# Kernel tuning notes

Measured on AMD Instinct MI355X. Metric: run time of the kernel, lower is better.

## Reference

```python
import jax, jax.numpy as jnp
import numpy as np

DIM = 4096; H = 32; D = 128; EPS = 1e-5
BLOCK = 16
BD = 8; MAXB = 64                    # decode seqs, blocks per decode seq
PB = 2; PSEQ = 1024; TP = PB * PSEQ  # prefill: 2 seqs x 1024 tokens
TOK = TP + BD
NBLOCKS = BD * MAXB + TP // BLOCK    # 640
NEG = -1e30


def setup_inputs() -> dict:
    key = jax.random.key(0)
    ks = jax.random.split(key, 10)
    std = 0.02
    x = jax.random.normal(ks[0], (TOK, DIM), jnp.float32)
    key_heap = jax.random.normal(ks[1], (NBLOCKS, BLOCK, H, D), jnp.float32)
    val_heap = jax.random.normal(ks[2], (NBLOCKS, BLOCK, H, D), jnp.float32)
    # decode seq i owns blocks [i*MAXB, (i+1)*MAXB); context_len includes the new token
    ctx = jax.random.randint(ks[3], (BD,), 256, MAXB * BLOCK + 1).astype(jnp.int32)
    block_table = (jnp.arange(BD)[:, None] * MAXB + jnp.arange(MAXB)[None, :]).astype(jnp.int32)
    prefill_slots = BD * MAXB * BLOCK + jnp.arange(TP)      # prefill fills blocks after decode region
    decode_slots = jnp.arange(BD) * MAXB * BLOCK + (ctx - 1)  # newest-token slot per decode seq
    slot_mapping = jnp.concatenate([prefill_slots, decode_slots]).astype(jnp.int32)
    cu = (jnp.arange(PB + 1) * PSEQ).astype(jnp.int32)
    return dict(
        x=x, key_heap=key_heap, val_heap=val_heap,
        slot_mapping=slot_mapping, decode_block_table=block_table,
        decode_context_lens=ctx, prefill_cu_seqlens=cu,
        num_prefill_tokens=TP, prefill_max_seqlen=PSEQ, decode_max_seq_len=MAXB * BLOCK,
        norm1_w=1.0 + std * jax.random.normal(ks[4], (DIM,), jnp.float32),
        norm2_w=1.0 + std * jax.random.normal(ks[5], (DIM,), jnp.float32),
        w_qkv_w=std * jax.random.normal(ks[6], (3 * H * D, DIM), jnp.float32),
        wo_w=std * jax.random.normal(ks[7], (DIM, H * D), jnp.float32),
        w_gate_up_w=std * jax.random.normal(ks[8], (8 * DIM, DIM), jnp.float32),
        w2_w=std * jax.random.normal(ks[9], (DIM, 4 * DIM), jnp.float32),
    )


def _rmsnorm(x, w):
    return x * jax.lax.rsqrt(jnp.mean(x * x, -1, keepdims=True) + EPS) * w


def _forward(x, key_heap, val_heap, norm1_w, norm2_w, w_qkv_w, wo_w, w_gate_up_w, w2_w,
             slot_mapping, decode_block_table, decode_context_lens, prefill_cu_seqlens,
             num_prefill_tokens):
    T = x.shape[0]
    scale = 1.0 / np.sqrt(D)
    residual = x
    # fused norm1 -> QKV projection
    qkv = (_rmsnorm(x, norm1_w) @ w_qkv_w.T).reshape(T, 3, H, D)
    q, k, v = qkv[:, 0], qkv[:, 1], qkv[:, 2]
    # paged cache write (ops.reshape_and_cache)
    nb, bs = key_heap.shape[0], key_heap.shape[1]
    key_flat = key_heap.reshape(nb * bs, H, D).at[slot_mapping].set(k)
    val_flat = val_heap.reshape(nb * bs, H, D).at[slot_mapping].set(v)
    # prefill: varlen causal self-attention (flash_attn_varlen_func)
    Tp = num_prefill_tokens
    pos = jnp.arange(Tp)
    seg = jnp.searchsorted(prefill_cu_seqlens, pos, side='right') - 1
    mask = (seg[:, None] == seg[None, :]) & (pos[:, None] >= pos[None, :])  # [Tp,Tp]
    s = jnp.einsum('ihd,jhd->hij', q[:Tp], k[:Tp]) * scale
    attn_p = jnp.einsum('hij,jhd->ihd',
                        jax.nn.softmax(jnp.where(mask[None], s, NEG), -1), v[:Tp])
    # decode: paged attention over cached KV (ops.paged_attention_v2)
    kd = key_flat.reshape(nb, bs, H, D)[decode_block_table].reshape(BD, -1, H, D)
    vd = val_flat.reshape(nb, bs, H, D)[decode_block_table].reshape(BD, -1, H, D)
    L = kd.shape[1]
    sd = jnp.einsum('bhd,blhd->bhl', q[Tp:], kd) * scale
    dmask = jnp.arange(L)[None, :] < decode_context_lens[:, None]
    attn_d = jnp.einsum('bhl,blhd->bhd',
                        jax.nn.softmax(jnp.where(dmask[:, None, :], sd, NEG), -1), vd)
    attn = jnp.concatenate([attn_p.reshape(Tp, H * D), attn_d.reshape(BD, H * D)], 0)
    # MLP: wo + residual, norm2, SwiGLU, down-proj, residual
    h = attn @ wo_w.T + residual
    residual = h
    gu = _rmsnorm(h, norm2_w) @ w_gate_up_w.T
    g, u = jnp.split(gu, 2, -1)
    return (jax.nn.silu(g) * u) @ w2_w.T + residual


def reference(x, key_heap, val_heap, slot_mapping, decode_block_table, decode_context_lens,
              prefill_cu_seqlens, num_prefill_tokens, prefill_max_seqlen, decode_max_seq_len,
              norm1_w, norm2_w, w_qkv_w, wo_w, w_gate_up_w, w2_w):
    del prefill_max_seqlen, decode_max_seq_len  # kernel scheduling hints only
    return _forward(x, key_heap, val_heap, norm1_w, norm2_w, w_qkv_w, wo_w, w_gate_up_w, w2_w,
                    slot_mapping, decode_block_table, decode_context_lens, prefill_cu_seqlens,
                    num_prefill_tokens)
```

## Files before the change

kernel.cpp:

```cpp
#include <hip/hip_runtime.h>
#include <hip/hip_bf16.h>
#include <stdint.h>

#define DIMC   4096
#define HC     32
#define DC     128
#define TPC    2048
#define TOKC   2056
#define BDC    8
#define MAXBC  64
#define PSEQC  1024
#define QKVN   12288
#define FFNC   16384
#define PSCALE 0.08838834764831843f

typedef __attribute__((ext_vector_type(8))) short short8;
typedef __attribute__((ext_vector_type(4))) float f32x4;
typedef __attribute__((ext_vector_type(4))) unsigned short u16x4;
typedef __attribute__((ext_vector_type(8))) unsigned short u16x8;

__device__ inline unsigned short f2bf(float f) {
  union { float f; unsigned u; } v; v.f = f;
  unsigned r = v.u + 0x7FFFu + ((v.u >> 16) & 1u);
  return (unsigned short)(r >> 16);
}
__device__ inline float bf2f(unsigned short u) {
  union { unsigned u; float f; } v; v.u = ((unsigned)u) << 16;
  return v.f;
}
__device__ inline f32x4 mfma16(short8 a, short8 b, f32x4 c) {
  return __builtin_amdgcn_mfma_f32_16x16x32_bf16(a, b, c, 0, 0, 0);
}
__device__ inline void gload16(const void* g, void* l) {
  __builtin_amdgcn_global_load_lds(
      (const __attribute__((address_space(1))) void*)g,
      (__attribute__((address_space(3))) void*)l, 16, 0, 0);
}

__global__ __launch_bounds__(256) void cvt_w(
    const float* __restrict__ in, unsigned short* __restrict__ out, long n8)
{
  long i = (long)blockIdx.x * 256 + threadIdx.x;
  const long stride = (long)gridDim.x * 256;
  for (; i < n8; i += stride) {
    f32x4 a = ((const f32x4*)in)[2 * i];
    f32x4 b = ((const f32x4*)in)[2 * i + 1];
    u16x8 o;
#pragma unroll
    for (int j = 0; j < 4; ++j) { o[j] = f2bf(a[j]); o[j + 4] = f2bf(b[j]); }
    ((u16x8*)out)[i] = o;
  }
}

__global__ __launch_bounds__(256) void rmsnorm_k(
    const float* __restrict__ x, const float* __restrict__ w,
    unsigned short* __restrict__ out)
{
  const int row = blockIdx.x;
  const int tid = threadIdx.x;
  const f32x4* xr = (const f32x4*)(x + (size_t)row * DIMC);
  f32x4 v[4];
  float ss = 0.f;
#pragma unroll
  for (int i = 0; i < 4; ++i) {
    v[i] = xr[i * 256 + tid];
    ss += v[i][0]*v[i][0] + v[i][1]*v[i][1] + v[i][2]*v[i][2] + v[i][3]*v[i][3];
  }
  for (int off = 32; off; off >>= 1) ss += __shfl_xor(ss, off);
  __shared__ float sred[4];
  if ((tid & 63) == 0) sred[tid >> 6] = ss;
  __syncthreads();
  const float rms = rsqrtf((sred[0]+sred[1]+sred[2]+sred[3]) * (1.f/DIMC) + 1e-5f);
  const f32x4* wr = (const f32x4*)w;
#pragma unroll
  for (int i = 0; i < 4; ++i) {
    f32x4 wv = wr[i * 256 + tid];
    u16x4 o;
#pragma unroll
    for (int j = 0; j < 4; ++j) o[j] = f2bf(v[i][j] * rms * wv[j]);
    *(u16x4*)(out + (size_t)row * DIMC + (size_t)(i * 256 + tid) * 4) = o;
  }
}

template<int MODE, int SK>
__global__ __launch_bounds__(512, 2) void gemm8p(
    const unsigned short* __restrict__ A, const unsigned short* __restrict__ Bh,
    float* __restrict__ Cf, unsigned short* __restrict__ Cb,
    const float* __restrict__ Res, int M, int N, int K)
{
  __shared__ char ldsc[131072];
  const int tid = threadIdx.x;
  const int lane = tid & 63, wid = tid >> 6;
  const int wr = wid >> 2, wc = wid & 3;
  const int lhi = lane >> 4, llo = lane & 15;

  const int nM = (M + 255) >> 8;
  const int nN = N >> 8;
  const int nwg = gridDim.x, orig = blockIdx.x;
  const int qq = nwg >> 3, rr = nwg & 7;
  const int xcd = orig & 7, lid = orig >> 3;
  const int wgid = (xcd < rr ? xcd*(qq+1) : rr*(qq+1) + (xcd-rr)*qq) + lid;
  const int tiles = nM * nN;
  const int ks = wgid / tiles;
  const int tile = wgid % tiles;
  const int bm = (tile % nM) << 8;
  const int bn = (tile / nM) << 8;
  const int kLen = K / SK;
  const int k0 = ks * kLen;
  const int NT = kLen >> 6;

  const unsigned short* src[2][2][2];
#pragma unroll
  for (int i = 0; i < 2; ++i) {
    int s = i * 512 + tid;
    int row = s >> 3;
    int chunk = (s & 7) ^ (row & 7);
#pragma unroll
    for (int h = 0; h < 2; ++h) {
      int ga = bm + h * 128 + row; ga = ga < M ? ga : M - 1;
      src[0][h][i] = A  + (size_t)ga * K + k0 + chunk * 8;
      src[1][h][i] = Bh + (size_t)(bn + h * 128 + row) * K + k0 + chunk * 8;
    }
  }

#define STG(U, OP, H) do { \
    int bb_ = (((U) & 1) << 16) + ((OP) << 15) + ((H) << 14) + (wid << 10); \
    gload16(src[OP][H][0] + ((size_t)(U) << 6), ldsc + bb_); \
    gload16(src[OP][H][1] + ((size_t)(U) << 6), ldsc + bb_ + 8192); \
  } while (0)

#define LDA(PB, HA) do { _Pragma("unroll") for (int m_ = 0; m_ < 4; ++m_) { \
    int row_ = wr*64 + m_*16 + llo; \
    int rb_ = (PB) + ((HA) << 14) + row_*128; int sx_ = (row_ & 7) << 4; \
    ar[m_][0] = *(const short8*)(ldsc + rb_ + ((lhi*16) ^ sx_)); \
    ar[m_][1] = *(const short8*)(ldsc + rb_ + ((64 + lhi*16) ^ sx_)); } } while (0)

#define LDB(PB, HB, DST) do { _Pragma("unroll") for (int n_ = 0; n_ < 2; ++n_) { \
    int row_ = wc*32 + n_*16 + llo; \
    int rb_ = (PB) + 32768 + ((HB) << 14) + row_*128; int sx_ = (row_ & 7) << 4; \
    DST[n_][0] = *(const short8*)(ldsc + rb_ + ((lhi*16) ^ sx_)); \
    DST[n_][1] = *(const short8*)(ldsc + rb_ + ((64 + lhi*16) ^ sx_)); } } while (0)

#define MM(QA, QB, B_) do { __builtin_amdgcn_s_setprio(1); \
    _Pragma("unroll") for (int m_ = 0; m_ < 4; ++m_) \
    _Pragma("unroll") for (int n_ = 0; n_ < 2; ++n_) { \
      acc[QA][QB][m_][n_] = mfma16(ar[m_][0], B_[n_][0], acc[QA][QB][m_][n_]); \
      acc[QA][QB][m_][n_] = mfma16(ar[m_][1], B_[n_][1], acc[QA][QB][m_][n_]); } \
    __builtin_amdgcn_s_setprio(0); } while (0)

#define FEN __builtin_amdgcn_sched_barrier(0)
#define BAR __builtin_amdgcn_s_barrier()
#define VMB(N) do { FEN; asm volatile("s_waitcnt vmcnt(" #N ")" ::: "memory"); \
    BAR; FEN; } while (0)

  f32x4 acc[2][2][4][2] = {};
  short8 ar[4][2], b0[2][2], b1[2][2];

  STG(0, 0, 0); STG(0, 1, 0); STG(0, 1, 1); STG(0, 0, 1);
  STG(1, 0, 0); STG(1, 1, 0); STG(1, 1, 1);
  VMB(6);
  LDA(0, 0); LDB(0, 0, b0);

  for (int t = 0; t < NT - 2; ++t) {
    const int pb = (t & 1) << 16, pbn = ((t + 1) & 1) << 16;
    LDB(pb, 1, b1);
    STG(t + 1, 0, 1);
    MM(0, 0, b0);
    BAR;
    STG(t + 2, 0, 0);
    MM(0, 1, b1);
    LDA(pb, 1);
    BAR;
    STG(t + 2, 1, 0);
    MM(1, 1, b1);
    VMB(8);
    STG(t + 2, 1, 1);
    MM(1, 0, b0);
    LDA(pbn, 0);
    LDB(pbn, 0, b0);
    VMB(6);
  }
  {
    const int pb = ((NT - 2) & 1) << 16, pbn = ((NT - 1) & 1) << 16;
    LDB(pb, 1, b1);
    STG(NT - 1, 0, 1);
    MM(0, 0, b0);
    BAR;
    MM(0, 1, b1);
    LDA(pb, 1);
    BAR;
    MM(1, 1, b1);
    VMB(4);
    MM(1, 0, b0);
    LDA(pbn, 0);
    LDB(pbn, 0, b0);
    VMB(0);
  }
  {
    const int pb = ((NT - 1) & 1) << 16;
    LDB(pb, 1, b1);
    MM(0, 0, b0);
    MM(0, 1, b1);
    LDA(pb, 1);
    MM(1, 1, b1);
    MM(1, 0, b0);
  }

  float* Pf = (MODE == 3) ? (Cf + (size_t)ks * M * N) : Cf;
#pragma unroll
  for (int qa = 0; qa < 2; ++qa)
#pragma unroll
  for (int m_ = 0; m_ < 4; ++m_)
#pragma unroll
  for (int j = 0; j < 4; ++j) {
    int row = bm + qa*128 + wr*64 + m_*16 + lhi*4 + j;
    if (row < M) {
#pragma unroll
      for (int qb = 0; qb < 2; ++qb)
#pragma unroll
      for (int n_ = 0; n_ < 2; ++n_) {
        int col = bn + qb*128 + wc*32 + n_*16 + llo;
        float v = acc[qa][qb][m_][n_][j];
        if (MODE == 1) { v += Res[(size_t)row*N + col]; Pf[(size_t)row*N + col] = v; }
        else if (MODE == 3) { Pf[(size_t)row*N + col] = v; }
        else Cb[(size_t)row*N + col] = f2bf(v);
      }
    }
  }
#undef STG
#undef LDA
#undef LDB
#undef MM
#undef FEN
#undef BAR
#undef VMB
}

__global__ __launch_bounds__(256) void redk(
    const float* __restrict__ p, const float* __restrict__ res,
    float* __restrict__ out, long n4)
{
  long i = (long)blockIdx.x * 256 + threadIdx.x;
  if (i >= n4) return;
  const f32x4* p4 = (const f32x4*)p;
  f32x4 v = p4[i] + p4[i + n4] + p4[i + 2*n4] + p4[i + 3*n4]
          + ((const f32x4*)res)[i];
  ((f32x4*)out)[i] = v;
}

template<int MODE, int BF16B>
__global__ __launch_bounds__(256) void gemm_bt(
    const unsigned short* __restrict__ A, const float* __restrict__ Bf,
    const unsigned short* __restrict__ Bh,
    float* __restrict__ Cf, unsigned short* __restrict__ Cb,
    const float* __restrict__ Res, int M, int N, int K)
{
  __shared__ unsigned short la[128 * 64];
  __shared__ unsigned short lb[128 * 64];
  const int tid = threadIdx.x;
  const int lane = tid & 63, wid = tid >> 6;
  const int wr = wid >> 1, wc = wid & 1;
  const int lhi = lane >> 4, llo = lane & 15;

  const int nM = (M + 127) >> 7;
  const int nwg = gridDim.x;
  const int orig = blockIdx.x;
  const int qq = nwg >> 3, rr = nwg & 7;
  const int xcd = orig & 7, lid = orig >> 3;
  const int wgid = (xcd < rr ? xcd * (qq + 1) : rr * (qq + 1) + (xcd - rr) * qq) + lid;
  const int bm = (wgid % nM) * 128;
  const int bn = (wgid / nM) * 128;

  const unsigned short* aSrc[4];
  const unsigned short* bSrcH[4];
  char* aDst[4];
  char* bDst[4];
#pragma unroll
  for (int p = 0; p < 4; ++p) {
    int slot = p * 256 + tid;
    int row = slot >> 3;
    int chunk = (slot & 7) ^ (row & 7);
    int gr = bm + row; gr = gr < M ? gr : M - 1;
    aSrc[p] = A + (size_t)gr * K + chunk * 8;
    aDst[p] = (char*)la + p * 4096 + wid * 1024;
    if (BF16B) {
      bSrcH[p] = Bh + (size_t)(bn + row) * K + chunk * 8;
      bDst[p] = (char*)lb + p * 4096 + wid * 1024;
    }
  }

  f32x4 acc[4][4] = {};

  for (int k0 = 0; k0 < K; k0 += 64) {
#pragma unroll
    for (int p = 0; p < 4; ++p) gload16(aSrc[p] + k0, aDst[p]);
    if (BF16B) {
#pragma unroll
      for (int p = 0; p < 4; ++p) gload16(bSrcH[p] + k0, bDst[p]);
    } else {
#pragma unroll
      for (int p = 0; p < 4; ++p) {
        int idx = p * 256 + tid;
        int row = idx >> 3, c8 = (idx & 7) << 3;
        const float* srcf = Bf + (size_t)(bn + row) * K + k0 + c8;
        f32x4 v0 = *(const f32x4*)srcf;
        f32x4 v1 = *(const f32x4*)(srcf + 4);
        short8 bv;
#pragma unroll
        for (int i = 0; i < 4; ++i) { bv[i] = (short)f2bf(v0[i]); bv[i+4] = (short)f2bf(v1[i]); }
        int byt = (row << 7) + (c8 << 1);
        byt ^= (row & 7) << 4;
        *(short8*)((char*)lb + byt) = bv;
      }
    }
    __syncthreads();
#pragma unroll
    for (int kk = 0; kk < 64; kk += 32) {
      short8 af[4], bfr[4];
#pragma unroll
      for (int m = 0; m < 4; ++m) {
        int row = wr * 64 + m * 16 + llo;
        int byt = (row << 7) + ((kk + lhi * 8) << 1);
        byt ^= (row & 7) << 4;
        af[m] = *(const short8*)((const char*)la + byt);
      }
#pragma unroll
      for (int n = 0; n < 4; ++n) {
        int row = wc * 64 + n * 16 + llo;
        int byt = (row << 7) + ((kk + lhi * 8) << 1);
        byt ^= (row & 7) << 4;
        bfr[n] = *(const short8*)((const char*)lb + byt);
      }
#pragma unroll
      for (int m = 0; m < 4; ++m)
#pragma unroll
        for (int n = 0; n < 4; ++n)
          acc[m][n] = mfma16(af[m], bfr[n], acc[m][n]);
    }
    __syncthreads();
  }

#pragma unroll
  for (int m = 0; m < 4; ++m) {
#pragma unroll
    for (int j = 0; j < 4; ++j) {
      int row = bm + wr * 64 + m * 16 + lhi * 4 + j;
      if (row < M) {
#pragma unroll
        for (int n = 0; n < 4; ++n) {
          int col = bn + wc * 64 + n * 16 + llo;
          float v = acc[m][n][j];
          if (MODE == 1) {
            v += Res[(size_t)row * N + col];
            Cf[(size_t)row * N + col] = v;
          } else {
            Cb[(size_t)row * N + col] = f2bf(v);
          }
        }
      }
    }
  }
}

__global__ __launch_bounds__(256) void prefill_attn(
    const unsigned short* __restrict__ qkv, unsigned short* __restrict__ attnb)
{
  const int h = blockIdx.x, qt = blockIdx.y, s = blockIdx.z;
  const int seq0 = s * PSEQC;
  const int q0 = qt * 64;
  const int tid = threadIdx.x;
  const int lane = tid & 63, w = tid >> 6;
  const int lhi = lane >> 4, llo = lane & 15;

  __shared__ unsigned short lk[64 * 128];
  __shared__ unsigned short lvt[128 * 72];
  __shared__ unsigned short lp[4][16 * 72];

  short8 qf[4];
  {
    const unsigned short* qrow =
        qkv + (size_t)(seq0 + q0 + w * 16 + llo) * QKVN + h * DC;
#pragma unroll
    for (int kk = 0; kk < 4; ++kk)
      qf[kk] = *(const short8*)(qrow + kk * 32 + lhi * 8);
  }

  float m_r[4], l_r[4];
#pragma unroll
  for (int r = 0; r < 4; ++r) { m_r[r] = -1e30f; l_r[r] = 0.f; }
  f32x4 oacc[8] = {};

  const int ntiles = qt + 1;
  for (int t = 0; t < ntiles; ++t) {
    const int j0 = t * 64;
#pragma unroll
    for (int p = 0; p < 4; ++p) {
      int idx = p * 256 + tid;
      int row = idx >> 4, c8 = (idx & 15) << 3;
      short8 kv = *(const short8*)(qkv + (size_t)(seq0 + j0 + row) * QKVN + DIMC + h * DC + c8);
      *(short8*)(lk + row * 128 + (c8 ^ ((row & 7) << 3))) = kv;
    }
#pragma unroll
    for (int p = 0; p < 4; ++p) {
      int idx = p * 256 + tid;
      int j = idx >> 4, c8 = (idx & 15) << 3;
      short8 vv = *(const short8*)(qkv + (size_t)(seq0 + j0 + j) * QKVN + 2 * DIMC + h * DC + c8);
#pragma unroll
      for (int i = 0; i < 8; ++i) {
        int d = c8 + i;
        int jj = j ^ (((d >> 3) & 7) << 3);
        lvt[d * 72 + jj] = (unsigned short)vv[i];
      }
    }
    __syncthreads();

    f32x4 sfr[4] = {};
#pragma unroll
    for (int n = 0; n < 4; ++n) {
      int row = n * 16 + llo;
#pragma unroll
      for (int kk = 0; kk < 4; ++kk) {
        int col = (kk * 32 + lhi * 8) ^ ((row & 7) << 3);
        short8 kf = *(const short8*)(lk + row * 128 + col);
        sfr[n] = mfma16(qf[kk], kf, sfr[n]);
      }
    }

    const bool diag = (t == ntiles - 1);
    const int qbase = q0 + w * 16 + lhi * 4;
    float pv[4][4];
#pragma unroll
    for (int r = 0; r < 4; ++r) {
      float mx = -1e30f;
#pragma unroll
      for (int n = 0; n < 4; ++n) {
        float sv = sfr[n][r] * PSCALE;
        if (diag && (j0 + n * 16 + llo > qbase + r)) sv = -1e30f;
        pv[n][r] = sv;
        mx = fmaxf(mx, sv);
      }
      for (int off = 8; off; off >>= 1) mx = fmaxf(mx, __shfl_xor(mx, off));
      float mnew = fmaxf(m_r[r], mx);
      float alpha = __expf(m_r[r] - mnew);
      m_r[r] = mnew;
      float rs = 0.f;
#pragma unroll
      for (int n = 0; n < 4; ++n) {
        float p = __expf(pv[n][r] - mnew);
        pv[n][r] = p;
        rs += p;
      }
      for (int off = 8; off; off >>= 1) rs += __shfl_xor(rs, off);
      l_r[r] = l_r[r] * alpha + rs;
#pragma unroll
      for (int f = 0; f < 8; ++f) oacc[f][r] *= alpha;
    }

    unsigned short* lpw = lp[w];
#pragma unroll
    for (int r = 0; r < 4; ++r)
#pragma unroll
      for (int n = 0; n < 4; ++n)
        lpw[(lhi * 4 + r) * 72 + n * 16 + llo] = f2bf(pv[n][r]);

#pragma unroll
    for (int kk = 0; kk < 2; ++kk) {
      short8 pf = *(const short8*)(lpw + llo * 72 + kk * 32 + lhi * 8);
#pragma unroll
      for (int f = 0; f < 8; ++f) {
        int d = f * 16 + llo;
        int jb = kk * 32 + lhi * 8;
        int jj = jb ^ (((d >> 3) & 7) << 3);
        short8 vf = *(const short8*)(lvt + d * 72 + jj);
        oacc[f] = mfma16(pf, vf, oacc[f]);
      }
    }
    __syncthreads();
  }

#pragma unroll
  for (int r = 0; r < 4; ++r) {
    int row = seq0 + q0 + w * 16 + lhi * 4 + r;
    float inv = 1.f / l_r[r];
#pragma unroll
    for (int f = 0; f < 8; ++f)
      attnb[(size_t)row * DIMC + h * DC + f * 16 + llo] = f2bf(oacc[f][r] * inv);
  }
}

__global__ __launch_bounds__(256) void decode_attn(
    const unsigned short* __restrict__ qkv,
    const float* __restrict__ kheap, const float* __restrict__ vheap,
    const int* __restrict__ btab, const int* __restrict__ ctxl,
    unsigned short* __restrict__ attnb)
{
  const int h = blockIdx.x, b = blockIdx.y;
  const int ctx = ctxl[b];
  const int tq = TPC + b;
  const int tid = threadIdx.x;
  __shared__ float sq[DC];
  __shared__ float sp[1024];
  __shared__ float sred[4];
  __shared__ float obuf[DC];

  const unsigned short* qrow = qkv + (size_t)tq * QKVN + h * DC;
  if (tid < DC) sq[tid] = bf2f(qrow[tid]);
  __syncthreads();

  float lmax = -1e30f;
#pragma unroll
  for (int i = 0; i < 4; ++i) {
    int l = i * 256 + tid;
    float sv = -1e30f;
    if (l < ctx) {
      float accd = 0.f;
      if (l == ctx - 1) {
        const unsigned short* kn = qkv + (size_t)tq * QKVN + DIMC + h * DC;
        for (int d = 0; d < DC; ++d) accd += sq[d] * bf2f(kn[d]);
      } else {
        int blk = btab[b * MAXBC + (l >> 4)];
        const float* kp = kheap + (((size_t)blk * 16 + (l & 15)) * HC + h) * DC;
#pragma unroll
        for (int d = 0; d < DC; d += 4) {
          f32x4 kv = *(const f32x4*)(kp + d);
          accd += sq[d] * kv[0] + sq[d+1] * kv[1] + sq[d+2] * kv[2] + sq[d+3] * kv[3];
        }
      }
      sv = accd * PSCALE;
    }
    sp[l] = sv;
    lmax = fmaxf(lmax, sv);
  }
  for (int off = 32; off; off >>= 1) lmax = fmaxf(lmax, __shfl_xor(lmax, off));
  if ((tid & 63) == 0) sred[tid >> 6] = lmax;
  __syncthreads();
  const float m = fmaxf(fmaxf(sred[0], sred[1]), fmaxf(sred[2], sred[3]));
  __syncthreads();

  float lsum = 0.f;
#pragma unroll
  for (int i = 0; i < 4; ++i) {
    int l = i * 256 + tid;
    float p = __expf(sp[l] - m);
    sp[l] = p;
    lsum += p;
  }
  for (int off = 32; off; off >>= 1) lsum += __shfl_xor(lsum, off);
  if ((tid & 63) == 0) sred[tid >> 6] = lsum;
  __syncthreads();
  const float denom = sred[0] + sred[1] + sred[2] + sred[3];

  const int d = tid & 127, half = tid >> 7;
  float o = 0.f;
  for (int l = half; l < ctx; l += 2) {
    float p = sp[l];
    float v;
    if (l == ctx - 1) {
      v = bf2f(qkv[(size_t)tq * QKVN + 2 * DIMC + h * DC + d]);
    } else {
      int blk = btab[b * MAXBC + (l >> 4)];
      v = vheap[(((size_t)blk * 16 + (l & 15)) * HC + h) * DC + d];
    }
    o += p * v;
  }
  if (half) obuf[d] = o;
  __syncthreads();
  if (!half)
    attnb[(size_t)tq * DIMC + h * DC + d] = f2bf((o + obuf[d]) / denom);
}

__global__ __launch_bounds__(256) void silu_mul(
    const unsigned short* __restrict__ gu, unsigned short* __restrict__ act)
{
  size_t chunk = (size_t)blockIdx.x * 256 + threadIdx.x;
  size_t row = chunk >> 11;
  int c = (int)(chunk & 2047) << 3;
  const unsigned short* g = gu + row * (2 * FFNC) + c;
  u16x8 gv = *(const u16x8*)g;
  u16x8 uv = *(const u16x8*)(g + FFNC);
  u16x8 o;
#pragma unroll
  for (int i = 0; i < 8; ++i) {
    float gf = bf2f(gv[i]);
    float uf = bf2f(uv[i]);
    float sf = gf / (1.f + __expf(-gf));
    o[i] = f2bf(sf * uf);
  }
  *(u16x8*)(act + row * FFNC + c) = o;
}

extern "C" void kernel_launch(void* const* d_in, const int* in_sizes, int n_in,
                              void* d_out, int out_size, void* d_ws, size_t ws_size,
                              hipStream_t stream) {
  const float* x     = (const float*)d_in[0];
  const float* kheap = (const float*)d_in[1];
  const float* vheap = (const float*)d_in[2];
  const int*   btab  = (const int*)d_in[4];
  const int*   ctxl  = (const int*)d_in[5];
  const float* n1w   = (const float*)d_in[10];
  const float* n2w   = (const float*)d_in[11];
  const float* wqkv  = (const float*)d_in[12];
  const float* wo    = (const float*)d_in[13];
  const float* wgu   = (const float*)d_in[14];
  const float* w2    = (const float*)d_in[15];
  float* out = (float*)d_out;

  char* ws = (char*)d_ws;
  unsigned short* xn   = (unsigned short*)(ws);
  unsigned short* qkvb = (unsigned short*)(ws + 16842752);
  unsigned short* actb = qkvb;
  unsigned short* attn = (unsigned short*)(ws + 16842752 + 67371008);
  float*          hbuf = (float*)(ws + 16842752 + 67371008 + 16842752);
  unsigned short* gub  = (unsigned short*)(ws + 16842752 + 67371008 + 16842752 + 33685504);

  const size_t wbase = 269484032;
  const bool bw = ws_size >= wbase + 536870912ull;
  unsigned short* wqkv_h = (unsigned short*)(ws + wbase);
  unsigned short* wo_h   = (unsigned short*)(ws + wbase + 100663296);
  unsigned short* wgu_h  = (unsigned short*)(ws + wbase + 100663296 + 33554432);
  unsigned short* w2_h   = (unsigned short*)(ws + wbase + 100663296 + 33554432 + 268435456);
  const size_t pko = wbase + 536870912ull;
  const bool sk4 = bw && (ws_size >= pko + 134742016ull);
  float* pbuf = (float*)(ws + pko);

  if (bw) {
    cvt_w<<<2048, 256, 0, stream>>>(wqkv, wqkv_h, (long)QKVN * DIMC / 8);
    cvt_w<<<2048, 256, 0, stream>>>(wo,   wo_h,   (long)DIMC * DIMC / 8);
    cvt_w<<<2048, 256, 0, stream>>>(wgu,  wgu_h,  (long)2 * FFNC * DIMC / 8);
    cvt_w<<<2048, 256, 0, stream>>>(w2,   w2_h,   (long)DIMC * FFNC / 8);
  }

  const int nM8 = 9;
  const int nM4 = 17;

  rmsnorm_k<<<TOKC, 256, 0, stream>>>(x, n1w, xn);
  if (bw) gemm8p<2,1><<<nM8 * (QKVN/256), 512, 0, stream>>>(xn, wqkv_h, nullptr, qkvb, nullptr, TOKC, QKVN, DIMC);
  else    gemm_bt<2,0><<<nM4 * (QKVN/128), 256, 0, stream>>>(xn, wqkv, nullptr, nullptr, qkvb, nullptr, TOKC, QKVN, DIMC);
  prefill_attn<<<dim3(HC, PSEQC / 64, 2), 256, 0, stream>>>(qkvb, attn);
  decode_attn<<<dim3(HC, BDC), 256, 0, stream>>>(qkvb, kheap, vheap, btab, ctxl, attn);
  if (bw) gemm_bt<1,1><<<nM4 * (DIMC/128), 256, 0, stream>>>(attn, nullptr, wo_h, hbuf, nullptr, x, TOKC, DIMC, DIMC);
  else    gemm_bt<1,0><<<nM4 * (DIMC/128), 256, 0, stream>>>(attn, wo, nullptr, hbuf, nullptr, x, TOKC, DIMC, DIMC);
  rmsnorm_k<<<TOKC, 256, 0, stream>>>(hbuf, n2w, xn);
  if (bw) gemm8p<2,1><<<nM8 * (2*FFNC/256), 512, 0, stream>>>(xn, wgu_h, nullptr, gub, nullptr, TOKC, 2*FFNC, DIMC);
  else    gemm_bt<2,0><<<nM4 * (2*FFNC/128), 256, 0, stream>>>(xn, wgu, nullptr, nullptr, gub, nullptr, TOKC, 2*FFNC, DIMC);
  silu_mul<<<(TOKC * (FFNC / 8)) / 256, 256, 0, stream>>>(gub, actb);
  if (sk4) {
    gemm8p<3,4><<<nM8 * (DIMC/256) * 4, 512, 0, stream>>>(actb, w2_h, pbuf, nullptr, nullptr, TOKC, DIMC, FFNC);
    redk<<<(TOKC * DIMC / 4 + 255) / 256, 256, 0, stream>>>(pbuf, hbuf, out, (long)TOKC * DIMC / 4);
  } else if (bw) {
    gemm8p<1,1><<<nM8 * (DIMC/256), 512, 0, stream>>>(actb, w2_h, out, nullptr, hbuf, TOKC, DIMC, FFNC);
  } else {
    gemm_bt<1,0><<<nM4 * (DIMC/128), 256, 0, stream>>>(actb, w2, nullptr, out, nullptr, hbuf, TOKC, DIMC, FFNC);
  }
}
```

Measured before the change: 1.901 ms.

## Widen prefill attention blocks to 128 queries with async K loads

Prefill attention now uses 512-thread blocks covering 128 query rows with 8 waves, so each K/V tile loaded into shared memory is reused by twice as many queries. K is loaded via a direct global-to-LDS path (gload16) with a swizzled source index, and V transposition writes pairs of rows as packed 32-bit stores. Waves whose query rows are entirely before the key tile skip compute while still participating in loads and barriers. The cost is fewer blocks (half the grid) and per-wave idle time on diagonal tiles, which may hurt occupancy and balance.

```diff
diff --git a/kernel.cpp b/kernel.cpp
--- a/kernel.cpp
+++ b/kernel.cpp
@@ -362,24 +362,25 @@
   }
 }
 
-__global__ __launch_bounds__(256) void prefill_attn(
+__global__ __launch_bounds__(512) void prefill_attn(
     const unsigned short* __restrict__ qkv, unsigned short* __restrict__ attnb)
 {
-  const int h = blockIdx.x, qt = blockIdx.y, s = blockIdx.z;
+  const int h = blockIdx.x, qtb = blockIdx.y, s = blockIdx.z;
   const int seq0 = s * PSEQC;
-  const int q0 = qt * 64;
+  const int q0 = qtb * 128;
   const int tid = threadIdx.x;
   const int lane = tid & 63, w = tid >> 6;
   const int lhi = lane >> 4, llo = lane & 15;
+  const int qw = q0 + w * 16;
 
   __shared__ unsigned short lk[64 * 128];
   __shared__ unsigned short lvt[128 * 72];
-  __shared__ unsigned short lp[4][16 * 72];
+  __shared__ unsigned short lp[8][16 * 72];
 
   short8 qf[4];
   {
     const unsigned short* qrow =
-        qkv + (size_t)(seq0 + q0 + w * 16 + llo) * QKVN + h * DC;
+        qkv + (size_t)(seq0 + qw + llo) * QKVN + h * DC;
 #pragma unroll
     for (int kk = 0; kk < 4; ++kk)
       qf[kk] = *(const short8*)(qrow + kk * 32 + lhi * 8);
@@ -390,89 +391,99 @@
   for (int r = 0; r < 4; ++r) { m_r[r] = -1e30f; l_r[r] = 0.f; }
   f32x4 oacc[8] = {};
 
-  const int ntiles = qt + 1;
+  const int ntiles = 2 * qtb + 2;
   for (int t = 0; t < ntiles; ++t) {
     const int j0 = t * 64;
 #pragma unroll
-    for (int p = 0; p < 4; ++p) {
-      int idx = p * 256 + tid;
-      int row = idx >> 4, c8 = (idx & 15) << 3;
-      short8 kv = *(const short8*)(qkv + (size_t)(seq0 + j0 + row) * QKVN + DIMC + h * DC + c8);
-      *(short8*)(lk + row * 128 + (c8 ^ ((row & 7) << 3))) = kv;
-    }
-#pragma unroll
-    for (int p = 0; p < 4; ++p) {
-      int idx = p * 256 + tid;
-      int j = idx >> 4, c8 = (idx & 15) << 3;
-      short8 vv = *(const short8*)(qkv + (size_t)(seq0 + j0 + j) * QKVN + 2 * DIMC + h * DC + c8);
+    for (int p = 0; p < 2; ++p) {
+      int idx = p * 512 + tid;
+      int row = idx >> 4, cs = idx & 15;
+      int cg = cs ^ (row & 7);
+      gload16(qkv + (size_t)(seq0 + j0 + row) * QKVN + DIMC + h * DC + cg * 8,
+              (char*)lk + p * 8192 + w * 1024);
+    }
+    {
+      int jp = tid >> 4;
+      int c8 = (tid & 15) << 3;
+      int j = jp * 2;
+      const unsigned short* vrow =
+          qkv + (size_t)(seq0 + j0 + j) * QKVN + 2 * DIMC + h * DC + c8;
+      short8 v0 = *(const short8*)vrow;
+      short8 v1 = *(const short8*)(vrow + QKVN);
 #pragma unroll
       for (int i = 0; i < 8; ++i) {
         int d = c8 + i;
         int jj = j ^ (((d >> 3) & 7) << 3);
-        lvt[d * 72 + jj] = (unsigned short)vv[i];
-      }
-    }
+        unsigned pack = (unsigned)(unsigned short)v0[i]
+                      | ((unsigned)(unsigned short)v1[i] << 16);
+        *(unsigned*)(lvt + d * 72 + jj) = pack;
+      }
+    }
+    asm volatile("s_waitcnt vmcnt(0)" ::: "memory");
     __syncthreads();
 
-    f32x4 sfr[4] = {};
-#pragma unroll
-    for (int n = 0; n < 4; ++n) {
-      int row = n * 16 + llo;
-#pragma unroll
-      for (int kk = 0; kk < 4; ++kk) {
-        int col = (kk * 32 + lhi * 8) ^ ((row & 7) << 3);
-        short8 kf = *(const short8*)(lk + row * 128 + col);
-        sfr[n] = mfma16(qf[kk], kf, sfr[n]);
-      }
-    }
-
-    const bool diag = (t == ntiles - 1);
-    const int qbase = q0 + w * 16 + lhi * 4;
-    float pv[4][4];
-#pragma unroll
-    for (int r = 0; r < 4; ++r) {
-      float mx = -1e30f;
+    const bool active = (j0 <= qw + 15);
+    if (active) {
+      f32x4 sfr[4] = {};
 #pragma unroll
       for (int n = 0; n < 4; ++n) {
-        float sv = sfr[n][r] * PSCALE;
-        if (diag && (j0 + n * 16 + llo > qbase + r)) sv = -1e30f;
-        pv[n][r] = sv;
-        mx = fmaxf(mx, sv);
-      }
-      for (int off = 8; off; off >>= 1) mx = fmaxf(mx, __shfl_xor(mx, off));
-      float mnew = fmaxf(m_r[r], mx);
-      float alpha = __expf(m_r[r] - mnew);
-      m_r[r] = mnew;
-      float rs = 0.f;
-#pragma unroll
-      for (int n = 0; n < 4; ++n) {
-        float p = __expf(pv[n][r] - mnew);
-        pv[n][r] = p;
-        rs += p;
-      }
-      for (int off = 8; off; off >>= 1) rs += __shfl_xor(rs, off);
-      l_r[r] = l_r[r] * alpha + rs;
-#pragma unroll
-      for (int f = 0; f < 8; ++f) oacc[f][r] *= alpha;
-    }
-
-    unsigned short* lpw = lp[w];
-#pragma unroll
-    for (int r = 0; r < 4; ++r)
-#pragma unroll
-      for (int n = 0; n < 4; ++n)
-        lpw[(lhi * 4 + r) * 72 + n * 16 + llo] = f2bf(pv[n][r]);
-
-#pragma unroll
-    for (int kk = 0; kk < 2; ++kk) {
-      short8 pf = *(const short8*)(lpw + llo * 72 + kk * 32 + lhi * 8);
-#pragma unroll
-      for (int f = 0; f < 8; ++f) {
-        int d = f * 16 + llo;
-        int jb = kk * 32 + lhi * 8;
-        int jj = jb ^ (((d >> 3) & 7) << 3);
-        short8 vf = *(const short8*)(lvt + d * 72 + jj);
-        oacc[f] = mfma16(pf, vf, oacc[f]);
+        int row = n * 16 + llo;
+#pragma unroll
+        for (int kk = 0; kk < 4; ++kk) {
+          int col = (kk * 32 + lhi * 8) ^ ((row & 7) << 3);
+          short8 kf = *(const short8*)(lk + row * 128 + col);
+          sfr[n] = mfma16(qf[kk], kf, sfr[n]);
+        }
+      }
+
+      const bool diag = (j0 + 63 > qw);
+      const int qbase = qw + lhi * 4;
+      float pv[4][4];
+#pragma unroll
+      for (int r = 0; r < 4; ++r) {
+        float mx = -1e30f;
+#pragma unroll
+        for (int n = 0; n < 4; ++n) {
+          float sv = sfr[n][r] * PSCALE;
+          if (diag && (j0 + n * 16 + llo > qbase + r)) sv = -1e30f;
+          pv[n][r] = sv;
+          mx = fmaxf(mx, sv);
+        }
+        for (int off = 8; off; off >>= 1) mx = fmaxf(mx, __shfl_xor(mx, off));
+        float mnew = fmaxf(m_r[r], mx);
+        float alpha = __expf(m_r[r] - mnew);
+        m_r[r] = mnew;
+        float rs = 0.f;
+#pragma unroll
+        for (int n = 0; n < 4; ++n) {
+          float p = __expf(pv[n][r] - mnew);
+          pv[n][r] = p;
+          rs += p;
+        }
+        for (int off = 8; off; off >>= 1) rs += __shfl_xor(rs, off);
+        l_r[r] = l_r[r] * alpha + rs;
+#pragma unroll
+        for (int f = 0; f < 8; ++f) oacc[f][r] *= alpha;
+      }
+
+      unsigned short* lpw = lp[w];
+#pragma unroll
+      for (int r = 0; r < 4; ++r)
+#pragma unroll
+        for (int n = 0; n < 4; ++n)
+          lpw[(lhi * 4 + r) * 72 + n * 16 + llo] = f2bf(pv[n][r]);
+
+#pragma unroll
+      for (int kk = 0; kk < 2; ++kk) {
+        short8 pf = *(const short8*)(lpw + llo * 72 + kk * 32 + lhi * 8);
+#pragma unroll
+        for (int f = 0; f < 8; ++f) {
+          int d = f * 16 + llo;
+          int jb = kk * 32 + lhi * 8;
+          int jj = jb ^ (((d >> 3) & 7) << 3);
+          short8 vf = *(const short8*)(lvt + d * 72 + jj);
+          oacc[f] = mfma16(pf, vf, oacc[f]);
+        }
       }
     }
     __syncthreads();
@@ -480,7 +491,7 @@
 
 #pragma unroll
   for (int r = 0; r < 4; ++r) {
-    int row = seq0 + q0 + w * 16 + lhi * 4 + r;
+    int row = seq0 + qw + lhi * 4 + r;
     float inv = 1.f / l_r[r];
 #pragma unroll
     for (int f = 0; f < 8; ++f)
@@ -636,7 +647,7 @@
   rmsnorm_k<<<TOKC, 256, 0, stream>>>(x, n1w, xn);
   if (bw) gemm8p<2,1><<<nM8 * (QKVN/256), 512, 0, stream>>>(xn, wqkv_h, nullptr, qkvb, nullptr, TOKC, QKVN, DIMC);
   else    gemm_bt<2,0><<<nM4 * (QKVN/128), 256, 0, stream>>>(xn, wqkv, nullptr, nullptr, qkvb, nullptr, TOKC, QKVN, DIMC);
-  prefill_attn<<<dim3(HC, PSEQC / 64, 2), 256, 0, stream>>>(qkvb, attn);
+  prefill_attn<<<dim3(HC, PSEQC / 128, 2), 512, 0, stream>>>(qkvb, attn);
   decode_attn<<<dim3(HC, BDC), 256, 0, stream>>>(qkvb, kheap, vheap, btab, ctxl, attn);
   if (bw) gemm_bt<1,1><<<nM4 * (DIMC/128), 256, 0, stream>>>(attn, nullptr, wo_h, hbuf, nullptr, x, TOKC, DIMC, DIMC);
   else    gemm_bt<1,0><<<nM4 * (DIMC/128), 256, 0, stream>>>(attn, wo, nullptr, hbuf, nullptr, x, TOKC, DIMC, DIMC);
```

New measurement: 1.901 ms. Within noise of the previous version (+0.0%).
